# Optimization experiments

Hardware: AMD Instinct MI355X
Metric: run time of the kernel (lower is better)

The kernel has to match this reference:

```python
import jax, jax.numpy as jnp
import numpy as np

N_FILTERS = 1024
N_HEADS = 16


def setup_inputs() -> dict:
    key = jax.random.key(0)
    k1, k2, k3 = jax.random.split(key, 3)
    x = jax.random.normal(k1, (8, 1024, N_FILTERS), dtype=jnp.float32)
    # VarianceScaling(0.02) ~ small dense init; 0.02*sqrt(1/fan_in) scale approximated
    w_qkv = jax.random.normal(k2, (N_FILTERS, N_FILTERS * 3), dtype=jnp.float32) * (0.02 / N_FILTERS) ** 0.5
    w_out = jax.random.normal(k3, (N_FILTERS, N_FILTERS), dtype=jnp.float32) * (0.02 / N_FILTERS) ** 0.5
    return {"x": x, "w_qkv": w_qkv, "w_out": w_out}


def reference(x, w_qkv, w_out):
    b, n, c = x.shape
    h = N_HEADS
    d = c // h
    qkv = jnp.einsum('bnc,ce->bne', x, w_qkv)  # [b, n, 3c]
    q, k, v = jnp.split(qkv, 3, axis=-1)
    # b n (h d) -> b h n d
    to_heads = lambda t: t.reshape(b, n, h, d).transpose(0, 2, 1, 3)
    q, k, v = to_heads(q), to_heads(k), to_heads(v)
    scale = jnp.sqrt(jnp.asarray(c, jnp.float32))  # NOTE: sqrt(n_filters), matches source
    attn = jnp.einsum('bhnd,bhmd->bhnm', q, k) / scale
    attn = jax.nn.softmax(attn, axis=-1)
    out = jnp.einsum('bhnm,bhmd->bhnd', attn, v)
    out = out.transpose(0, 2, 1, 3).reshape(b, n, c)  # b h n d -> b n (h d)
    return jnp.einsum('bnc,co->bno', out, w_out)
```

## Files before the change

kernel.cpp:

```cpp
#include <hip/hip_runtime.h>
#include <hip/hip_bf16.h>

typedef __bf16 bf16_t;
typedef __bf16 bf16x8 __attribute__((ext_vector_type(8)));
typedef __bf16 bf16x4 __attribute__((ext_vector_type(4)));
typedef float f32x4 __attribute__((ext_vector_type(4)));

constexpr int LD = 3072;

#define MFMA_16x16x32(a, b, c) __builtin_amdgcn_mfma_f32_16x16x32_bf16((a), (b), (c), 0, 0, 0)

#define GLOAD_LDS16(g, l)                                               \
  __builtin_amdgcn_global_load_lds(                                     \
      (const __attribute__((address_space(1))) void*)(g),               \
      (__attribute__((address_space(3))) void*)(l), 16, 0, 0)

#define TRREAD(dst, addr, imm) \
  asm volatile("ds_read_b64_tr_b16 %0, %1 offset:" imm : "=v"(dst) : "v"(addr))

#define BAR __builtin_amdgcn_s_barrier()
#define LGKM0 do { asm volatile("s_waitcnt lgkmcnt(0)" ::: "memory"); \
                   __builtin_amdgcn_sched_barrier(0); } while (0)

__global__ void cvt_kernel(const float* __restrict__ in, bf16_t* __restrict__ out, int n8) {
  int i = blockIdx.x * blockDim.x + threadIdx.x;
  if (i >= n8) return;
  const float4 a = reinterpret_cast<const float4*>(in)[2 * i];
  const float4 c = reinterpret_cast<const float4*>(in)[2 * i + 1];
  bf16x8 o;
  o[0] = (bf16_t)a.x; o[1] = (bf16_t)a.y; o[2] = (bf16_t)a.z; o[3] = (bf16_t)a.w;
  o[4] = (bf16_t)c.x; o[5] = (bf16_t)c.y; o[6] = (bf16_t)c.z; o[7] = (bf16_t)c.w;
  reinterpret_cast<bf16x8*>(out)[i] = o;
}

__global__ void tcvt_kernel(const float* __restrict__ in, bf16_t* __restrict__ out, int R, int C) {
  __shared__ float tile[32][33];
  const int c0 = blockIdx.x * 32, r0 = blockIdx.y * 32;
  const int tx = threadIdx.x & 31, ty = threadIdx.x >> 5;
#pragma unroll
  for (int i = 0; i < 32; i += 8)
    tile[ty + i][tx] = in[(size_t)(r0 + ty + i) * C + (c0 + tx)];
  __syncthreads();
#pragma unroll
  for (int i = 0; i < 32; i += 8)
    out[(size_t)(c0 + ty + i) * R + (r0 + tx)] = (bf16_t)tile[tx][ty + i];
}

__global__ __launch_bounds__(512, 2) void gemm_qkv_256(
    const bf16_t* __restrict__ A, const bf16_t* __restrict__ Bt,
    bf16_t* __restrict__ C, float q_scale) {
  constexpr int K = 1024;
  extern __shared__ char smem[];
  char* asB = smem;
  char* bsB = smem + 65536;

  const int t = threadIdx.x;
  const int lane = t & 63, wave = t >> 6;
  const int l15 = lane & 15, lg = lane >> 4;
  const int wr = wave >> 2, wc = wave & 3;

  const int bid = blockIdx.x;
  const int wg = (bid & 7) * 48 + (bid >> 3);
  const int brow = (wg & 31) * 256;
  const int bcol = (wg >> 5) * 256;

  const int srow = t >> 3;
  const int schk = (t & 7) ^ (srow & 7);
  const bf16_t* aS = A + (size_t)(brow + srow) * K + schk * 8;
  const bf16_t* bS = Bt + (size_t)(bcol + srow) * K + schk * 8;
  const int ldst = t * 8;

#define STG_A(T, H) do {                                                      \
    const bf16_t* _s = aS + (size_t)((H) * 128) * K + (T) * 64;               \
    bf16_t* _d = (bf16_t*)(asB + ((T) & 1) * 32768 + (H) * 16384) + ldst;     \
    GLOAD_LDS16(_s, _d);                                                      \
    GLOAD_LDS16(_s + (size_t)64 * K, _d + 4096);                              \
  } while (0)
#define STG_B(T, H) do {                                                      \
    const bf16_t* _s = bS + (size_t)((H) * 128) * K + (T) * 64;               \
    bf16_t* _d = (bf16_t*)(bsB + ((T) & 1) * 32768 + (H) * 16384) + ldst;     \
    GLOAD_LDS16(_s, _d);                                                      \
    GLOAD_LDS16(_s + (size_t)64 * K, _d + 4096);                              \
  } while (0)

  const int rx = l15 & 7;
  const unsigned c0 = ((unsigned)(lg ^ rx)) << 4;
  const unsigned c1 = ((unsigned)((4 | lg) ^ rx)) << 4;
  const unsigned a_rd = (unsigned)(wr * 16384 + l15 * 128);
  const unsigned b_rd = (unsigned)((wc >> 1) * 16384 + (wc & 1) * 8192 + l15 * 128);

  f32x4 acc[8][4] = {};
  bf16x8 af[4][2], bfr[2][2];

#define RD_AF(BUF, MH) do { _Pragma("unroll")                                 \
    for (int m = 0; m < 4; ++m) {                                             \
      const char* _p = asB + (BUF) * 32768 + a_rd + ((MH) * 4 + m) * 2048;    \
      af[m][0] = *(const bf16x8*)(_p + c0);                                   \
      af[m][1] = *(const bf16x8*)(_p + c1); } } while (0)
#define RD_BF(BUF, NH) do { _Pragma("unroll")                                 \
    for (int n = 0; n < 2; ++n) {                                             \
      const char* _p = bsB + (BUF) * 32768 + b_rd + ((NH) * 2 + n) * 2048;    \
      bfr[n][0] = *(const bf16x8*)(_p + c0);                                  \
      bfr[n][1] = *(const bf16x8*)(_p + c1); } } while (0)
#define MM16(MH, NH) do {                                                     \
    __builtin_amdgcn_s_setprio(1);                                            \
    _Pragma("unroll")                                                         \
    for (int m = 0; m < 4; ++m) { _Pragma("unroll")                           \
      for (int n = 0; n < 2; ++n) {                                           \
        acc[(MH)*4+m][(NH)*2+n] =                                             \
            MFMA_16x16x32(af[m][0], bfr[n][0], acc[(MH)*4+m][(NH)*2+n]);      \
        acc[(MH)*4+m][(NH)*2+n] =                                             \
            MFMA_16x16x32(af[m][1], bfr[n][1], acc[(MH)*4+m][(NH)*2+n]); } }  \
    __builtin_amdgcn_s_setprio(0); } while (0)

  STG_A(0, 0); STG_A(0, 1); STG_B(0, 0); STG_B(0, 1); STG_A(1, 0);
  asm volatile("s_waitcnt vmcnt(2)" ::: "memory");
  BAR;

  for (int i = 0; i < 8; ++i) {
    const int T1 = 2 * i + 1, T2 = 2 * i + 2, T3 = 2 * i + 3;
    const bool pf = (i < 7);
    STG_A(T1, 1);
    RD_AF(0, 0); RD_BF(0, 0);
    BAR; LGKM0; MM16(0, 0); BAR;
    STG_B(T1, 0);
    RD_BF(0, 1);
    BAR; LGKM0; MM16(0, 1); BAR;
    STG_B(T1, 1);
    RD_AF(0, 1);
    BAR; LGKM0; MM16(1, 1); BAR;
    if (pf) STG_A(T2, 0);
    RD_BF(0, 0);
    BAR; LGKM0; MM16(1, 0);
    if (pf) asm volatile("s_waitcnt vmcnt(2)" ::: "memory");
    else    asm volatile("s_waitcnt vmcnt(0)" ::: "memory");
    BAR;
    if (pf) STG_A(T2, 1);
    RD_AF(1, 0); RD_BF(1, 0);
    BAR; LGKM0; MM16(0, 0); BAR;
    if (pf) STG_B(T2, 0);
    RD_BF(1, 1);
    BAR; LGKM0; MM16(0, 1); BAR;
    if (pf) STG_B(T2, 1);
    RD_AF(1, 1);
    BAR; LGKM0; MM16(1, 1); BAR;
    if (pf) STG_A(T3, 0);
    RD_BF(1, 0);
    BAR; LGKM0; MM16(1, 0);
    asm volatile("s_waitcnt vmcnt(2)" ::: "memory");
    BAR;
  }

  const float sc = (bcol < 1024) ? q_scale : 1.0f;
  const int crow0 = brow + wr * 128 + lg * 4;
  const int ccol0 = bcol + wc * 64 + l15;
#pragma unroll
  for (int m = 0; m < 8; ++m)
#pragma unroll
    for (int n = 0; n < 4; ++n)
#pragma unroll
      for (int r = 0; r < 4; ++r)
        C[(size_t)(crow0 + m * 16 + r) * 3072 + ccol0 + n * 16] =
            (bf16_t)(acc[m][n][r] * sc);
#undef STG_A
#undef STG_B
#undef RD_AF
#undef RD_BF
#undef MM16
}

template <typename OutT>
__global__ __launch_bounds__(256) void gemm_bt_kernel(
    const bf16_t* __restrict__ A, const bf16_t* __restrict__ Bt, OutT* __restrict__ C,
    int M, int N, int K, int q_cols, float q_scale) {
  __shared__ bf16_t As[2][4096];
  __shared__ bf16_t Bs[2][4096];
  const int tid = threadIdx.x;
  const int lane = tid & 63;
  const int wave = tid >> 6;
  const int l15 = lane & 15, lg = lane >> 4;
  const int wr = wave >> 1, wc = wave & 1;
  const int brow = blockIdx.y * 128, bcol = blockIdx.x * 128;

  f32x4 acc[4][4] = {};

  const int srow = tid >> 2;
  const int scol = (tid & 3) * 8;
  const bf16_t* Ag = A + (size_t)(brow + srow) * K + scol;
  const bf16_t* Bg = Bt + (size_t)(bcol + srow) * K + scol;

  {
    bf16_t* aw = &As[0][wave * 512];
    bf16_t* bw = &Bs[0][wave * 512];
    GLOAD_LDS16(Ag, aw);
    GLOAD_LDS16(Ag + (size_t)64 * K, aw + 2048);
    GLOAD_LDS16(Bg, bw);
    GLOAD_LDS16(Bg + (size_t)64 * K, bw + 2048);
  }
  __syncthreads();

  const int nsteps = K >> 5;
  for (int i = 0; i < nsteps; i++) {
    if (i + 1 < nsteps) {
      const int k0 = (i + 1) << 5;
      bf16_t* aw = &As[(i + 1) & 1][wave * 512];
      bf16_t* bw = &Bs[(i + 1) & 1][wave * 512];
      GLOAD_LDS16(Ag + k0, aw);
      GLOAD_LDS16(Ag + k0 + (size_t)64 * K, aw + 2048);
      GLOAD_LDS16(Bg + k0, bw);
      GLOAD_LDS16(Bg + k0 + (size_t)64 * K, bw + 2048);
    }
    const bf16_t* as = As[i & 1];
    const bf16_t* bs = Bs[i & 1];
    bf16x8 af[4], bfr[4];
#pragma unroll
    for (int j = 0; j < 4; j++)
      af[j] = *reinterpret_cast<const bf16x8*>(as + (wr * 64 + j * 16 + l15) * 32 + lg * 8);
#pragma unroll
    for (int j = 0; j < 4; j++)
      bfr[j] = *reinterpret_cast<const bf16x8*>(bs + (wc * 64 + j * 16 + l15) * 32 + lg * 8);
#pragma unroll
    for (int j = 0; j < 4; j++)
#pragma unroll
      for (int k = 0; k < 4; k++)
        acc[j][k] = MFMA_16x16x32(af[j], bfr[k], acc[j][k]);
    __syncthreads();
  }

  const float sc = (bcol < q_cols) ? q_scale : 1.0f;
#pragma unroll
  for (int i = 0; i < 4; i++)
#pragma unroll
    for (int j = 0; j < 4; j++)
#pragma unroll
      for (int r = 0; r < 4; r++) {
        const size_t row = (size_t)(brow + wr * 64 + i * 16 + lg * 4 + r);
        const size_t col = (size_t)(bcol + wc * 64 + j * 16 + l15);
        C[row * N + col] = (OutT)(acc[i][j][r] * sc);
      }
}

__device__ __forceinline__ unsigned pack_bf16_pair(float a, float b) {
  union { __hip_bfloat162 h; unsigned u; } c;
  c.h = __float22bfloat162_rn(float2{a, b});
  return c.u;
}

__global__ __launch_bounds__(256, 3) void attn_kernel(const bf16_t* __restrict__ qkv,
                                                      bf16_t* __restrict__ ctx) {
  __shared__ bf16_t Ks[2][4096];
  __shared__ bf16_t Vs[2][4096];
  const int tid = threadIdx.x, lane = tid & 63, wave = tid >> 6;
  const int l15 = lane & 15, lg = (lane >> 4) & 3;
  const int flat = blockIdx.x;
  const int xcd = flat & 7, rr = flat >> 3;
  const int qt = rr & 7;
  const int hb = xcd * 16 + (rr >> 3);
  const int h = hb & 15, b = hb >> 4;
  const size_t base = (size_t)b * 1024 * LD;
  const int qbase = qt * 128 + wave * 32;

  bf16x8 qa[2][2];
#pragma unroll
  for (int s = 0; s < 2; s++) {
    const bf16_t* qp = qkv + base + (size_t)(qbase + s * 16 + l15) * LD + h * 64 + lg * 8;
    qa[s][0] = *reinterpret_cast<const bf16x8*>(qp);
    qa[s][1] = *reinterpret_cast<const bf16x8*>(qp + 32);
  }

  const bf16_t* Kb = qkv + base + 1024 + h * 64;
  const bf16_t* Vb = qkv + base + 2048 + h * 64;

  const int krr = lane >> 3;
  const int kcc = (lane & 7) ^ krr;
  const bf16_t* ksrc0 = Kb + (size_t)(wave * 16 + krr) * LD + kcc * 8;
  const bf16_t* ksrc1 = ksrc0 + (size_t)8 * LD;

  const int vd0 = (lane & 1) * 8 + wave * 16;
  const int vkv = ((lane >> 1) & 3) + ((lane >> 3) & 3) * 4 + (lane >> 5) * 16;
  const bf16_t* vsrc0 = Vb + (size_t)vkv * LD + vd0;
  const bf16_t* vsrc1 = vsrc0 + (size_t)32 * LD;

  bf16_t* ksb = &Ks[0][0];
  bf16_t* vsb = &Vs[0][0];
  const char* ksr = (const char*)&Ks[0][0];
  const unsigned vs_byte =
      (unsigned)(size_t)(__attribute__((address_space(3))) void*)(&Vs[0][0]);
  const unsigned tr_lane = vs_byte + lane * 8;

  const int rx7 = l15 & 7;
  const unsigned kb0 = (unsigned)(l15 * 128 + ((lg ^ rx7) << 4));
  const unsigned kb1 = (unsigned)(l15 * 128 + (((4 | lg) ^ rx7) << 4));

  float lr[2] = {0.f, 0.f};
  f32x4 oacc[2][4] = {};

  GLOAD_LDS16(ksrc0, ksb + wave * 1024);
  GLOAD_LDS16(ksrc1, ksb + wave * 1024 + 512);
  GLOAD_LDS16(vsrc0, vsb + wave * 1024);
  GLOAD_LDS16(vsrc1, vsb + wave * 1024 + 512);
  ksrc0 += (size_t)64 * LD; ksrc1 += (size_t)64 * LD;
  vsrc0 += (size_t)64 * LD; vsrc1 += (size_t)64 * LD;
  __syncthreads();

  for (int t = 0; t < 16; t++) {
    const int cur = t & 1;
    if (t < 15) {
      bf16_t* kd = ksb + (cur ^ 1) * 4096 + wave * 1024;
      bf16_t* vd = vsb + (cur ^ 1) * 4096 + wave * 1024;
      GLOAD_LDS16(ksrc0, kd);
      GLOAD_LDS16(ksrc1, kd + 512);
      GLOAD_LDS16(vsrc0, vd);
      GLOAD_LDS16(vsrc1, vd + 512);
      ksrc0 += (size_t)64 * LD; ksrc1 += (size_t)64 * LD;
      vsrc0 += (size_t)64 * LD; vsrc1 += (size_t)64 * LD;
    }

    f32x4 sacc[2][4] = {};
    const char* kt = ksr + cur * 8192;
    __builtin_amdgcn_s_setprio(1);
#pragma unroll
    for (int tt = 0; tt < 4; tt++) {
      const bf16x8 k0 = *reinterpret_cast<const bf16x8*>(kt + tt * 2048 + kb0);
      const bf16x8 k1 = *reinterpret_cast<const bf16x8*>(kt + tt * 2048 + kb1);
      sacc[0][tt] = MFMA_16x16x32(k0, qa[0][0], sacc[0][tt]);
      sacc[0][tt] = MFMA_16x16x32(k1, qa[0][1], sacc[0][tt]);
      sacc[1][tt] = MFMA_16x16x32(k0, qa[1][0], sacc[1][tt]);
      sacc[1][tt] = MFMA_16x16x32(k1, qa[1][1], sacc[1][tt]);
    }
    __builtin_amdgcn_s_setprio(0);

    const unsigned ta = tr_lane + (unsigned)cur * 8192;
    bf16x4 tl0, th0, tl2, th2, tl4, th4, tl6, th6;
    TRREAD(tl0, ta, "0");    TRREAD(th0, ta, "512");
    TRREAD(tl2, ta, "2048"); TRREAD(th2, ta, "2560");
    TRREAD(tl4, ta, "4096"); TRREAD(th4, ta, "4608");
    TRREAD(tl6, ta, "6144"); TRREAD(th6, ta, "6656");
    __builtin_amdgcn_sched_barrier(0);

    unsigned pu[16];
    float ls0 = 0.f, ls1 = 0.f;
#pragma unroll
    for (int tt = 0; tt < 4; tt++) {
      const float a0 = __builtin_exp2f(sacc[0][tt][0]);
      const float a1 = __builtin_exp2f(sacc[0][tt][1]);
      const float a2 = __builtin_exp2f(sacc[0][tt][2]);
      const float a3 = __builtin_exp2f(sacc[0][tt][3]);
      ls0 += (a0 + a1) + (a2 + a3);
      pu[(tt >> 1) * 4 + (tt & 1) * 2 + 0] = pack_bf16_pair(a0, a1);
      pu[(tt >> 1) * 4 + (tt & 1) * 2 + 1] = pack_bf16_pair(a2, a3);
      const float b0 = __builtin_exp2f(sacc[1][tt][0]);
      const float b1 = __builtin_exp2f(sacc[1][tt][1]);
      const float b2 = __builtin_exp2f(sacc[1][tt][2]);
      const float b3 = __builtin_exp2f(sacc[1][tt][3]);
      ls1 += (b0 + b1) + (b2 + b3);
      pu[8 + (tt >> 1) * 4 + (tt & 1) * 2 + 0] = pack_bf16_pair(b0, b1);
      pu[8 + (tt >> 1) * 4 + (tt & 1) * 2 + 1] = pack_bf16_pair(b2, b3);
    }
    lr[0] += ls0;
    lr[1] += ls1;
    bf16x8 pa[2][2];
    pa[0][0] = *reinterpret_cast<bf16x8*>(&pu[0]);
    pa[0][1] = *reinterpret_cast<bf16x8*>(&pu[4]);
    pa[1][0] = *reinterpret_cast<bf16x8*>(&pu[8]);
    pa[1][1] = *reinterpret_cast<bf16x8*>(&pu[12]);

    bf16x4 tl1, th1, tl3, th3, tl5, th5, tl7, th7;
    TRREAD(tl1, ta, "1024"); TRREAD(th1, ta, "1536");
    TRREAD(tl3, ta, "3072"); TRREAD(th3, ta, "3584");
    TRREAD(tl5, ta, "5120"); TRREAD(th5, ta, "5632");
    TRREAD(tl7, ta, "7168"); TRREAD(th7, ta, "7680");

    asm volatile("s_waitcnt lgkmcnt(8)" ::: "memory");
    __builtin_amdgcn_sched_barrier(0);
    {
      bf16x8 vb0[4];
      vb0[0] = __builtin_shufflevector(tl0, th0, 0, 1, 2, 3, 4, 5, 6, 7);
      vb0[1] = __builtin_shufflevector(tl2, th2, 0, 1, 2, 3, 4, 5, 6, 7);
      vb0[2] = __builtin_shufflevector(tl4, th4, 0, 1, 2, 3, 4, 5, 6, 7);
      vb0[3] = __builtin_shufflevector(tl6, th6, 0, 1, 2, 3, 4, 5, 6, 7);
      __builtin_amdgcn_s_setprio(1);
#pragma unroll
      for (int s = 0; s < 2; s++)
#pragma unroll
        for (int dt = 0; dt < 4; dt++)
          oacc[s][dt] = MFMA_16x16x32(pa[s][0], vb0[dt], oacc[s][dt]);
      __builtin_amdgcn_s_setprio(0);
    }

    asm volatile("s_waitcnt lgkmcnt(0)" ::: "memory");
    __builtin_amdgcn_sched_barrier(0);
    {
      bf16x8 vb1[4];
      vb1[0] = __builtin_shufflevector(tl1, th1, 0, 1, 2, 3, 4, 5, 6, 7);
      vb1[1] = __builtin_shufflevector(tl3, th3, 0, 1, 2, 3, 4, 5, 6, 7);
      vb1[2] = __builtin_shufflevector(tl5, th5, 0, 1, 2, 3, 4, 5, 6, 7);
      vb1[3] = __builtin_shufflevector(tl7, th7, 0, 1, 2, 3, 4, 5, 6, 7);
      __builtin_amdgcn_s_setprio(1);
#pragma unroll
      for (int s = 0; s < 2; s++)
#pragma unroll
        for (int dt = 0; dt < 4; dt++)
          oacc[s][dt] = MFMA_16x16x32(pa[s][1], vb1[dt], oacc[s][dt]);
      __builtin_amdgcn_s_setprio(0);
    }

    __syncthreads();
  }

#pragma unroll
  for (int s = 0; s < 2; s++) {
    float v = lr[s];
    v += __shfl_xor(v, 16);
    v += __shfl_xor(v, 32);
#pragma unroll
    for (int r = 0; r < 4; r++) {
      const float inv = 1.0f / __shfl(v, lg * 4 + r);
      const size_t row = (size_t)(b * 1024 + qbase + s * 16 + lg * 4 + r);
#pragma unroll
      for (int dt = 0; dt < 4; dt++)
        ctx[row * 1024 + h * 64 + dt * 16 + l15] = (bf16_t)(oacc[s][dt][r] * inv);
    }
  }
}

extern "C" void kernel_launch(void* const* d_in, const int* in_sizes, int n_in,
                              void* d_out, int out_size, void* d_ws, size_t ws_size,
                              hipStream_t stream) {
  (void)in_sizes; (void)n_in; (void)out_size; (void)ws_size;
  const float* x = (const float*)d_in[0];
  const float* w_qkv = (const float*)d_in[1];
  const float* w_out = (const float*)d_in[2];
  float* out = (float*)d_out;
  char* ws = (char*)d_ws;

  bf16_t* x_b   = (bf16_t*)(ws);
  bf16_t* qkv_b = (bf16_t*)(ws + (size_t)(16 << 20));
  bf16_t* wqT   = (bf16_t*)(ws + (size_t)(64 << 20));
  bf16_t* woT   = (bf16_t*)(ws + (size_t)(70 << 20));
  bf16_t* ctx_b = (bf16_t*)(ws + (size_t)(72 << 20));

  const float qsc = 0.045084220027780106f;

  cvt_kernel<<<8388608 / 8 / 256, 256, 0, stream>>>(x, x_b, 8388608 / 8);
  tcvt_kernel<<<dim3(3072 / 32, 1024 / 32), 256, 0, stream>>>(w_qkv, wqT, 1024, 3072);
  tcvt_kernel<<<dim3(1024 / 32, 1024 / 32), 256, 0, stream>>>(w_out, woT, 1024, 1024);

  gemm_qkv_256<<<384, 512, 131072, stream>>>(x_b, wqT, qkv_b, qsc);
  attn_kernel<<<1024, 256, 0, stream>>>(qkv_b, ctx_b);
  gemm_bt_kernel<float><<<dim3(1024 / 128, 8192 / 128), 256, 0, stream>>>(
      ctx_b, woT, out, 8192, 1024, 1024, 0, 1.0f);
}
```

Measured before the change: 169.9 us.

## Process two KV tiles per iteration with software-pipelined QK, softmax and PV

```diff
diff --git a/kernel.cpp b/kernel.cpp
--- a/kernel.cpp
+++ b/kernel.cpp
@@ -248,8 +248,8 @@
 
 __global__ __launch_bounds__(256, 3) void attn_kernel(const bf16_t* __restrict__ qkv,
                                                       bf16_t* __restrict__ ctx) {
-  __shared__ bf16_t Ks[2][4096];
-  __shared__ bf16_t Vs[2][4096];
+  __shared__ bf16_t Ks[2][8192];
+  __shared__ bf16_t Vs[2][8192];
   const int tid = threadIdx.x, lane = tid & 63, wave = tid >> 6;
   const int l15 = lane & 15, lg = (lane >> 4) & 3;
   const int flat = blockIdx.x;
@@ -275,7 +275,6 @@
   const int kcc = (lane & 7) ^ krr;
   const bf16_t* ksrc0 = Kb + (size_t)(wave * 16 + krr) * LD + kcc * 8;
   const bf16_t* ksrc1 = ksrc0 + (size_t)8 * LD;
-
   const int vd0 = (lane & 1) * 8 + wave * 16;
   const int vkv = ((lane >> 1) & 3) + ((lane >> 3) & 3) * 4 + (lane >> 5) * 16;
   const bf16_t* vsrc0 = Vb + (size_t)vkv * LD + vd0;
@@ -295,115 +294,143 @@
   float lr[2] = {0.f, 0.f};
   f32x4 oacc[2][4] = {};
 
-  GLOAD_LDS16(ksrc0, ksb + wave * 1024);
-  GLOAD_LDS16(ksrc1, ksb + wave * 1024 + 512);
-  GLOAD_LDS16(vsrc0, vsb + wave * 1024);
-  GLOAD_LDS16(vsrc1, vsb + wave * 1024 + 512);
-  ksrc0 += (size_t)64 * LD; ksrc1 += (size_t)64 * LD;
-  vsrc0 += (size_t)64 * LD; vsrc1 += (size_t)64 * LD;
+#define STAGE_PAIR(PB, KV0) do {                                         \
+    const size_t _go = (size_t)(KV0) * LD;                               \
+    const size_t _g1 = _go + (size_t)64 * LD;                            \
+    bf16_t* _kd = ksb + (PB) * 8192 + wave * 1024;                       \
+    bf16_t* _vd = vsb + (PB) * 8192 + wave * 1024;                       \
+    GLOAD_LDS16(ksrc0 + _go, _kd);                                       \
+    GLOAD_LDS16(ksrc1 + _go, _kd + 512);                                 \
+    GLOAD_LDS16(ksrc0 + _g1, _kd + 4096);                                \
+    GLOAD_LDS16(ksrc1 + _g1, _kd + 4096 + 512);                          \
+    GLOAD_LDS16(vsrc0 + _go, _vd);                                       \
+    GLOAD_LDS16(vsrc1 + _go, _vd + 512);                                 \
+    GLOAD_LDS16(vsrc0 + _g1, _vd + 4096);                                \
+    GLOAD_LDS16(vsrc1 + _g1, _vd + 4096 + 512);                          \
+  } while (0)
+
+#define SOFTMAX(SACC, PA) do {                                           \
+    unsigned _pu[16];                                                    \
+    float _l0 = 0.f, _l1 = 0.f;                                          \
+    _Pragma("unroll")                                                    \
+    for (int tt = 0; tt < 4; tt++) {                                     \
+      const float a0 = __builtin_exp2f(SACC[0][tt][0]);                  \
+      const float a1 = __builtin_exp2f(SACC[0][tt][1]);                  \
+      const float a2 = __builtin_exp2f(SACC[0][tt][2]);                  \
+      const float a3 = __builtin_exp2f(SACC[0][tt][3]);                  \
+      _l0 += (a0 + a1) + (a2 + a3);                                      \
+      _pu[(tt >> 1) * 4 + (tt & 1) * 2 + 0] = pack_bf16_pair(a0, a1);    \
+      _pu[(tt >> 1) * 4 + (tt & 1) * 2 + 1] = pack_bf16_pair(a2, a3);    \
+      const float b0 = __builtin_exp2f(SACC[1][tt][0]);                  \
+      const float b1 = __builtin_exp2f(SACC[1][tt][1]);                  \
+      const float b2 = __builtin_exp2f(SACC[1][tt][2]);                  \
+      const float b3 = __builtin_exp2f(SACC[1][tt][3]);                  \
+      _l1 += (b0 + b1) + (b2 + b3);                                      \
+      _pu[8 + (tt >> 1) * 4 + (tt & 1) * 2 + 0] = pack_bf16_pair(b0, b1);\
+      _pu[8 + (tt >> 1) * 4 + (tt & 1) * 2 + 1] = pack_bf16_pair(b2, b3);\
+    }                                                                    \
+    lr[0] += _l0; lr[1] += _l1;                                          \
+    PA[0][0] = *reinterpret_cast<bf16x8*>(&_pu[0]);                      \
+    PA[0][1] = *reinterpret_cast<bf16x8*>(&_pu[4]);                      \
+    PA[1][0] = *reinterpret_cast<bf16x8*>(&_pu[8]);                      \
+    PA[1][1] = *reinterpret_cast<bf16x8*>(&_pu[12]);                     \
+  } while (0)
+
+#define TR16(TA, P)                                                      \
+  bf16x4 P##l0, P##h0, P##l1, P##h1, P##l2, P##h2, P##l3, P##h3,         \
+         P##l4, P##h4, P##l5, P##h5, P##l6, P##h6, P##l7, P##h7;         \
+  TRREAD(P##l0, TA, "0");    TRREAD(P##h0, TA, "512");                   \
+  TRREAD(P##l1, TA, "1024"); TRREAD(P##h1, TA, "1536");                  \
+  TRREAD(P##l2, TA, "2048"); TRREAD(P##h2, TA, "2560");                  \
+  TRREAD(P##l3, TA, "3072"); TRREAD(P##h3, TA, "3584");                  \
+  TRREAD(P##l4, TA, "4096"); TRREAD(P##h4, TA, "4608");                  \
+  TRREAD(P##l5, TA, "5120"); TRREAD(P##h5, TA, "5632");                  \
+  TRREAD(P##l6, TA, "6144"); TRREAD(P##h6, TA, "6656");                  \
+  TRREAD(P##l7, TA, "7168"); TRREAD(P##h7, TA, "7680");
+
+#define VBUILD(P, VB) do {                                               \
+    VB[0][0] = __builtin_shufflevector(P##l0, P##h0, 0,1,2,3,4,5,6,7);   \
+    VB[1][0] = __builtin_shufflevector(P##l1, P##h1, 0,1,2,3,4,5,6,7);   \
+    VB[0][1] = __builtin_shufflevector(P##l2, P##h2, 0,1,2,3,4,5,6,7);   \
+    VB[1][1] = __builtin_shufflevector(P##l3, P##h3, 0,1,2,3,4,5,6,7);   \
+    VB[0][2] = __builtin_shufflevector(P##l4, P##h4, 0,1,2,3,4,5,6,7);   \
+    VB[1][2] = __builtin_shufflevector(P##l5, P##h5, 0,1,2,3,4,5,6,7);   \
+    VB[0][3] = __builtin_shufflevector(P##l6, P##h6, 0,1,2,3,4,5,6,7);   \
+    VB[1][3] = __builtin_shufflevector(P##l7, P##h7, 0,1,2,3,4,5,6,7);   \
+  } while (0)
+
+#define PV(PA, VB) do { _Pragma("unroll")                                \
+    for (int s = 0; s < 2; s++) { _Pragma("unroll")                      \
+      for (int dt = 0; dt < 4; dt++) {                                   \
+        oacc[s][dt] = MFMA_16x16x32(PA[s][0], VB[0][dt], oacc[s][dt]);   \
+        oacc[s][dt] = MFMA_16x16x32(PA[s][1], VB[1][dt], oacc[s][dt]);   \
+      } } } while (0)
+
+  STAGE_PAIR(0, 0);
   __syncthreads();
 
-  for (int t = 0; t < 16; t++) {
-    const int cur = t & 1;
-    if (t < 15) {
-      bf16_t* kd = ksb + (cur ^ 1) * 4096 + wave * 1024;
-      bf16_t* vd = vsb + (cur ^ 1) * 4096 + wave * 1024;
-      GLOAD_LDS16(ksrc0, kd);
-      GLOAD_LDS16(ksrc1, kd + 512);
-      GLOAD_LDS16(vsrc0, vd);
-      GLOAD_LDS16(vsrc1, vd + 512);
-      ksrc0 += (size_t)64 * LD; ksrc1 += (size_t)64 * LD;
-      vsrc0 += (size_t)64 * LD; vsrc1 += (size_t)64 * LD;
-    }
-
-    f32x4 sacc[2][4] = {};
-    const char* kt = ksr + cur * 8192;
-    __builtin_amdgcn_s_setprio(1);
-#pragma unroll
-    for (int tt = 0; tt < 4; tt++) {
-      const bf16x8 k0 = *reinterpret_cast<const bf16x8*>(kt + tt * 2048 + kb0);
-      const bf16x8 k1 = *reinterpret_cast<const bf16x8*>(kt + tt * 2048 + kb1);
-      sacc[0][tt] = MFMA_16x16x32(k0, qa[0][0], sacc[0][tt]);
-      sacc[0][tt] = MFMA_16x16x32(k1, qa[0][1], sacc[0][tt]);
-      sacc[1][tt] = MFMA_16x16x32(k0, qa[1][0], sacc[1][tt]);
-      sacc[1][tt] = MFMA_16x16x32(k1, qa[1][1], sacc[1][tt]);
-    }
-    __builtin_amdgcn_s_setprio(0);
-
-    const unsigned ta = tr_lane + (unsigned)cur * 8192;
-    bf16x4 tl0, th0, tl2, th2, tl4, th4, tl6, th6;
-    TRREAD(tl0, ta, "0");    TRREAD(th0, ta, "512");
-    TRREAD(tl2, ta, "2048"); TRREAD(th2, ta, "2560");
-    TRREAD(tl4, ta, "4096"); TRREAD(th4, ta, "4608");
-    TRREAD(tl6, ta, "6144"); TRREAD(th6, ta, "6656");
-    __builtin_amdgcn_sched_barrier(0);
-
-    unsigned pu[16];
-    float ls0 = 0.f, ls1 = 0.f;
-#pragma unroll
-    for (int tt = 0; tt < 4; tt++) {
-      const float a0 = __builtin_exp2f(sacc[0][tt][0]);
-      const float a1 = __builtin_exp2f(sacc[0][tt][1]);
-      const float a2 = __builtin_exp2f(sacc[0][tt][2]);
-      const float a3 = __builtin_exp2f(sacc[0][tt][3]);
-      ls0 += (a0 + a1) + (a2 + a3);
-      pu[(tt >> 1) * 4 + (tt & 1) * 2 + 0] = pack_bf16_pair(a0, a1);
-      pu[(tt >> 1) * 4 + (tt & 1) * 2 + 1] = pack_bf16_pair(a2, a3);
-      const float b0 = __builtin_exp2f(sacc[1][tt][0]);
-      const float b1 = __builtin_exp2f(sacc[1][tt][1]);
-      const float b2 = __builtin_exp2f(sacc[1][tt][2]);
-      const float b3 = __builtin_exp2f(sacc[1][tt][3]);
-      ls1 += (b0 + b1) + (b2 + b3);
-      pu[8 + (tt >> 1) * 4 + (tt & 1) * 2 + 0] = pack_bf16_pair(b0, b1);
-      pu[8 + (tt >> 1) * 4 + (tt & 1) * 2 + 1] = pack_bf16_pair(b2, b3);
-    }
-    lr[0] += ls0;
-    lr[1] += ls1;
-    bf16x8 pa[2][2];
-    pa[0][0] = *reinterpret_cast<bf16x8*>(&pu[0]);
-    pa[0][1] = *reinterpret_cast<bf16x8*>(&pu[4]);
-    pa[1][0] = *reinterpret_cast<bf16x8*>(&pu[8]);
-    pa[1][1] = *reinterpret_cast<bf16x8*>(&pu[12]);
-
-    bf16x4 tl1, th1, tl3, th3, tl5, th5, tl7, th7;
-    TRREAD(tl1, ta, "1024"); TRREAD(th1, ta, "1536");
-    TRREAD(tl3, ta, "3072"); TRREAD(th3, ta, "3584");
-    TRREAD(tl5, ta, "5120"); TRREAD(th5, ta, "5632");
-    TRREAD(tl7, ta, "7168"); TRREAD(th7, ta, "7680");
-
-    asm volatile("s_waitcnt lgkmcnt(8)" ::: "memory");
-    __builtin_amdgcn_sched_barrier(0);
+  for (int j = 0; j < 8; j++) {
+    const int pb = j & 1;
+    if (j < 7) STAGE_PAIR(pb ^ 1, (j + 1) * 128);
+
+    const unsigned pbyte = (unsigned)pb * 16384;
+
+    f32x4 sA[2][4] = {};
     {
-      bf16x8 vb0[4];
-      vb0[0] = __builtin_shufflevector(tl0, th0, 0, 1, 2, 3, 4, 5, 6, 7);
-      vb0[1] = __builtin_shufflevector(tl2, th2, 0, 1, 2, 3, 4, 5, 6, 7);
-      vb0[2] = __builtin_shufflevector(tl4, th4, 0, 1, 2, 3, 4, 5, 6, 7);
-      vb0[3] = __builtin_shufflevector(tl6, th6, 0, 1, 2, 3, 4, 5, 6, 7);
+      const char* kt = ksr + pbyte;
       __builtin_amdgcn_s_setprio(1);
 #pragma unroll
-      for (int s = 0; s < 2; s++)
-#pragma unroll
-        for (int dt = 0; dt < 4; dt++)
-          oacc[s][dt] = MFMA_16x16x32(pa[s][0], vb0[dt], oacc[s][dt]);
+      for (int tt = 0; tt < 4; tt++) {
+        const bf16x8 k0 = *reinterpret_cast<const bf16x8*>(kt + tt * 2048 + kb0);
+        const bf16x8 k1 = *reinterpret_cast<const bf16x8*>(kt + tt * 2048 + kb1);
+        sA[0][tt] = MFMA_16x16x32(k0, qa[0][0], sA[0][tt]);
+        sA[0][tt] = MFMA_16x16x32(k1, qa[0][1], sA[0][tt]);
+        sA[1][tt] = MFMA_16x16x32(k0, qa[1][0], sA[1][tt]);
+        sA[1][tt] = MFMA_16x16x32(k1, qa[1][1], sA[1][tt]);
+      }
       __builtin_amdgcn_s_setprio(0);
     }
 
-    asm volatile("s_waitcnt lgkmcnt(0)" ::: "memory");
-    __builtin_amdgcn_sched_barrier(0);
+    const unsigned taA = tr_lane + pbyte;
+    TR16(taA, ta_);
+    bf16x8 kB[4][2];
     {
-      bf16x8 vb1[4];
-      vb1[0] = __builtin_shufflevector(tl1, th1, 0, 1, 2, 3, 4, 5, 6, 7);
-      vb1[1] = __builtin_shufflevector(tl3, th3, 0, 1, 2, 3, 4, 5, 6, 7);
-      vb1[2] = __builtin_shufflevector(tl5, th5, 0, 1, 2, 3, 4, 5, 6, 7);
-      vb1[3] = __builtin_shufflevector(tl7, th7, 0, 1, 2, 3, 4, 5, 6, 7);
-      __builtin_amdgcn_s_setprio(1);
-#pragma unroll
-      for (int s = 0; s < 2; s++)
-#pragma unroll
-        for (int dt = 0; dt < 4; dt++)
-          oacc[s][dt] = MFMA_16x16x32(pa[s][1], vb1[dt], oacc[s][dt]);
-      __builtin_amdgcn_s_setprio(0);
+      const char* kt = ksr + pbyte + 8192;
+#pragma unroll
+      for (int tt = 0; tt < 4; tt++) {
+        kB[tt][0] = *reinterpret_cast<const bf16x8*>(kt + tt * 2048 + kb0);
+        kB[tt][1] = *reinterpret_cast<const bf16x8*>(kt + tt * 2048 + kb1);
+      }
     }
+    LGKM0;
+
+    f32x4 sB[2][4] = {};
+#pragma unroll
+    for (int tt = 0; tt < 4; tt++) {
+      sB[0][tt] = MFMA_16x16x32(kB[tt][0], qa[0][0], sB[0][tt]);
+      sB[0][tt] = MFMA_16x16x32(kB[tt][1], qa[0][1], sB[0][tt]);
+      sB[1][tt] = MFMA_16x16x32(kB[tt][0], qa[1][0], sB[1][tt]);
+      sB[1][tt] = MFMA_16x16x32(kB[tt][1], qa[1][1], sB[1][tt]);
+    }
+    bf16x8 paA[2][2];
+    SOFTMAX(sA, paA);
+
+    const unsigned taB = taA + 8192;
+    TR16(taB, tb_);
+
+    bf16x8 vbA[2][4];
+    VBUILD(ta_, vbA);
+    PV(paA, vbA);
+    bf16x8 paB[2][2];
+    SOFTMAX(sB, paB);
+
+    LGKM0;
+
+    bf16x8 vbB[2][4];
+    VBUILD(tb_, vbB);
+    __builtin_amdgcn_s_setprio(1);
+    PV(paB, vbB);
+    __builtin_amdgcn_s_setprio(0);
 
     __syncthreads();
   }
@@ -422,6 +449,11 @@
         ctx[row * 1024 + h * 64 + dt * 16 + l15] = (bf16_t)(oacc[s][dt][r] * inv);
     }
   }
+#undef STAGE_PAIR
+#undef SOFTMAX
+#undef TR16
+#undef VBUILD
+#undef PV
 }
 
 extern "C" void kernel_launch(void* const* d_in, const int* in_sizes, int n_in,
```

New measurement: 176.0 us. +3.6%, slower.
